# Kernel optimization log

Measured on AMD Instinct MI355X. Metric: run time of the kernel, lower is better.

## Reference

```python
import jax, jax.numpy as jnp
import numpy as np

HEAD_DIM = 64
GRID = 4
DS = 4
EPS = 1e-6


def conv1x1(x, w, b):
    # x: (B,C,H,W), w: (O,C), b: (O,)
    return jnp.einsum('bchw,oc->bohw', x, w) + b[None, :, None, None]


def setup_inputs() -> dict:
    key = jax.random.key(0)
    ks = jax.random.split(key, 12)
    B, N, C = 16, 4096, 256
    s = 0.02
    return {
        'x': jax.random.normal(ks[0], (B, N, C), dtype=jnp.float32),
        'w_qkv': s * jax.random.normal(ks[1], (3 * C, C), dtype=jnp.float32),
        'b_qkv': jnp.zeros((3 * C,), dtype=jnp.float32),
        'w_q': s * jax.random.normal(ks[2], (C, C), dtype=jnp.float32),
        'b_q': jnp.zeros((C,), dtype=jnp.float32),
        'w_kv': s * jax.random.normal(ks[3], (2 * C, C), dtype=jnp.float32),
        'b_kv': jnp.zeros((2 * C,), dtype=jnp.float32),
        'w_proj': s * jax.random.normal(ks[4], (C, C), dtype=jnp.float32),
        'b_proj': jnp.zeros((C,), dtype=jnp.float32),
        'gn_w': jnp.ones((C,), dtype=jnp.float32),
        'gn_b': jnp.zeros((C,), dtype=jnp.float32),
    }


def reference(x, w_qkv, b_qkv, w_q, b_q, w_kv, b_kv, w_proj, b_proj, gn_w, gn_b):
    B, N, C = x.shape
    H = W = int(np.sqrt(N))
    hd = HEAD_DIM
    nh = C // hd
    gs = GRID
    scale = hd ** -0.5

    xi = x.transpose(0, 2, 1).reshape(B, C, H, W)
    qkv = conv1x1(xi, w_qkv, b_qkv)  # (B,3C,H,W)

    # ---- grid-window attention (gs x gs windows) ----
    gh, gw = H // gs, W // gs
    qkv = qkv.reshape(B, 3, nh, hd, gh, gs, gw, gs)
    qkv = qkv.transpose(1, 0, 2, 4, 6, 5, 7, 3).reshape(3, -1, gs * gs, hd)
    q, k, v = qkv[0], qkv[1], qkv[2]  # (B*nh*gh*gw, gs*gs, hd)
    attn = jax.nn.softmax(jnp.einsum('wqd,wkd->wqk', q, k) * scale, axis=-1)
    grid_x = jnp.einsum('wqk,wkd->wqd', attn, v)
    grid_x = grid_x.reshape(B, nh, gh, gw, gs, gs, hd)
    grid_x = grid_x.transpose(0, 1, 6, 2, 4, 3, 5).reshape(B, C, H, W)

    # channels_first LayerNorm(x + grid_x)
    z = xi + grid_x
    u = z.mean(1, keepdims=True)
    s2 = ((z - u) ** 2).mean(1, keepdims=True)
    grid_x = gn_w[None, :, None, None] * ((z - u) / jnp.sqrt(s2 + EPS)) + gn_b[None, :, None, None]

    # ---- pooled global attention ----
    qg = conv1x1(grid_x, w_q, b_q).reshape(B, nh, hd, N).transpose(0, 1, 3, 2)  # (B,nh,N,hd)
    pooled = grid_x.reshape(B, C, H // DS, DS, W // DS, DS).mean(axis=(3, 5))
    kv = conv1x1(pooled, w_kv, b_kv).reshape(B, 2, nh, hd, -1).transpose(1, 0, 2, 4, 3)
    k, v = kv[0], kv[1]  # (B,nh,Np,hd)
    attn = jax.nn.softmax(jnp.einsum('bhqd,bhkd->bhqk', qg, k) * scale, axis=-1)
    global_x = jnp.einsum('bhqk,bhkd->bhqd', attn, v)
    global_x = global_x.transpose(0, 1, 3, 2).reshape(B, C, H, W) + grid_x

    out = conv1x1(global_x, w_proj, b_proj)
    return out.reshape(B, C, N).transpose(0, 2, 1)
```

## Files before the change

### kernel.cpp

```cpp
#include <hip/hip_runtime.h>
#include <cstddef>

#define SCALE 0.125f
#define LN_EPS 1e-6f

typedef __attribute__((ext_vector_type(8))) short bf16x8;
typedef __attribute__((ext_vector_type(4))) float f32x4;

__device__ __forceinline__ unsigned short f2bf(float f) {
    unsigned u = __float_as_uint(f);
    return (unsigned short)((u + 0x7FFFu + ((u >> 16) & 1u)) >> 16);
}
__device__ __forceinline__ unsigned pack2(float a, float b) {
    return (unsigned)f2bf(a) | ((unsigned)f2bf(b) << 16);
}
__device__ __forceinline__ float bf2f(short s) { return __uint_as_float(((unsigned)(unsigned short)s) << 16); }

#define GLOAD16(gp, lp) __builtin_amdgcn_global_load_lds( \
    (const __attribute__((address_space(1))) void*)(gp),  \
    (__attribute__((address_space(3))) void*)(lp), 16, 0, 0)

__global__ __launch_bounds__(256) void k_castw(
    const float* __restrict__ wqkv, const float* __restrict__ wq,
    const float* __restrict__ wkv, const float* __restrict__ wproj,
    short* __restrict__ wb)
{
    const int blk = blockIdx.x;
    const float* src; size_t so, doff;
    if (blk < 96)       { src = wqkv;  so = (size_t)blk * 2048;         doff = 0; }
    else if (blk < 128) { src = wq;    so = (size_t)(blk - 96) * 2048;  doff = 196608; }
    else if (blk < 192) { src = wkv;   so = (size_t)(blk - 128) * 2048; doff = 262144; }
    else                { src = wproj; so = (size_t)(blk - 192) * 2048; doff = 393216; }
    const size_t idx = so + (size_t)threadIdx.x * 8;
    const float4 f0 = *(const float4*)(src + idx);
    const float4 f1 = *(const float4*)(src + idx + 4);
    uint4 o;
    o.x = pack2(f0.x, f0.y); o.y = pack2(f0.z, f0.w);
    o.z = pack2(f1.x, f1.y); o.w = pack2(f1.z, f1.w);
    *(uint4*)(wb + doff + idx) = o;
}

__global__ __launch_bounds__(256) void k_castx(
    const float* __restrict__ x, short* __restrict__ xb)
{
    const size_t i = ((size_t)blockIdx.x * 256 + threadIdx.x) * 8;
    const float4 f0 = *(const float4*)(x + i);
    const float4 f1 = *(const float4*)(x + i + 4);
    uint4 o;
    o.x = pack2(f0.x, f0.y); o.y = pack2(f0.z, f0.w);
    o.z = pack2(f1.x, f1.y); o.w = pack2(f1.z, f1.w);
    *(uint4*)(xb + i) = o;
}

template<int OUTMODE>
__global__ __launch_bounds__(256, 4) void k_gemm(
    const short* __restrict__ Asrc, const short* __restrict__ Bw,
    const float* __restrict__ bias, void* __restrict__ Cdst,
    short* __restrict__ Vdst, int ldc, int nbn)
{
    __shared__ short Sh[17408];
    short* const As0 = Sh;
    short* const Bs0 = Sh + 8192;

    const int tid = threadIdx.x;
    const int q8 = gridDim.x >> 3;
    const int bid = (blockIdx.x & 7) * q8 + (blockIdx.x >> 3);
    const int bm = bid / nbn, bn = bid % nbn;
    const size_t m0 = (size_t)bm * 128, n0 = (size_t)bn * 128;
    const int wid = tid >> 6, lane = tid & 63;
    const int wr = wid >> 1, wc = wid & 1;
    const int g = lane >> 4, r = lane & 15;
    const int rowc = lane >> 3, gran = lane & 7;

    f32x4 acc[4][4];
    #pragma unroll
    for (int mi = 0; mi < 4; ++mi)
        #pragma unroll
        for (int nj = 0; nj < 4; ++nj) acc[mi][nj] = (f32x4)0.f;

    auto STAGE = [&](int kt) {
        const int k0 = kt * 64;
        #pragma unroll
        for (int i = 0; i < 4; ++i) {
            const int rbase = wid * 32 + i * 8;
            const int row = rbase + rowc;
            const int sg = gran ^ (row & 7);
            GLOAD16(Asrc + (m0 + row) * 256 + k0 + sg * 8, As0 + rbase * 64);
            GLOAD16(Bw   + (n0 + row) * 256 + k0 + sg * 8, Bs0 + rbase * 64);
        }
    };

    auto COMPUTE = [&]() {
        #pragma unroll
        for (int ks = 0; ks < 2; ++ks) {
            const int ke = ks * 32 + g * 8;
            bf16x8 a[4], b[4];
            #pragma unroll
            for (int mi = 0; mi < 4; ++mi) {
                const int row = wr * 64 + mi * 16 + r;
                a[mi] = *(const bf16x8*)&As0[row * 64 + (ke ^ ((row & 7) << 3))];
            }
            #pragma unroll
            for (int nj = 0; nj < 4; ++nj) {
                const int row = wc * 64 + nj * 16 + r;
                b[nj] = *(const bf16x8*)&Bs0[row * 64 + (ke ^ ((row & 7) << 3))];
            }
            #pragma unroll
            for (int mi = 0; mi < 4; ++mi)
                #pragma unroll
                for (int nj = 0; nj < 4; ++nj)
                    acc[mi][nj] = __builtin_amdgcn_mfma_f32_16x16x32_bf16(
                        a[mi], b[nj], acc[mi][nj], 0, 0, 0);
        }
    };

    #pragma unroll
    for (int kt = 0; kt < 4; ++kt) {
        STAGE(kt);
        __syncthreads();
        COMPUTE();
        __syncthreads();
    }

    if (OUTMODE == 1) {
        short* const Cl = Sh;
        #pragma unroll
        for (int nj = 0; nj < 4; ++nj) {
            const int col = wc * 64 + nj * 16 + r;
            const float bv = bias[n0 + col];
            #pragma unroll
            for (int mi = 0; mi < 4; ++mi) {
                const int row = wr * 64 + mi * 16 + g * 4;
                #pragma unroll
                for (int e = 0; e < 4; ++e)
                    Cl[(row + e) * 136 + col] = (short)f2bf(acc[mi][nj][e] + bv);
            }
        }
        __syncthreads();
        short* C = (short*)Cdst;
        #pragma unroll
        for (int j = 0; j < 8; ++j) {
            const int row = j * 16 + (tid >> 4);
            const int c8 = (tid & 15) * 8;
            const uint4 v = *(const uint4*)&Cl[row * 136 + c8];
            *(uint4*)(C + (m0 + row) * ldc + n0 + c8) = v;
        }
    } else if (OUTMODE == 0) {
        float* const Clf = (float*)Sh;
        float* C = (float*)Cdst;
        #pragma unroll
        for (int p = 0; p < 2; ++p) {
            if (wr == p) {
                #pragma unroll
                for (int nj = 0; nj < 4; ++nj) {
                    const int col = wc * 64 + nj * 16 + r;
                    const float bv = bias[n0 + col];
                    #pragma unroll
                    for (int mi = 0; mi < 4; ++mi) {
                        const int lrow = mi * 16 + g * 4;
                        #pragma unroll
                        for (int e = 0; e < 4; ++e)
                            Clf[(lrow + e) * 132 + col] = acc[mi][nj][e] + bv;
                    }
                }
            }
            __syncthreads();
            #pragma unroll
            for (int j = 0; j < 8; ++j) {
                const int lin = j * 256 + tid;
                const int row = lin >> 5, c4 = (lin & 31) * 4;
                const float4 v = *(const float4*)&Clf[row * 132 + c4];
                *(float4*)(C + (m0 + p * 64 + row) * ldc + n0 + c4) = v;
            }
            __syncthreads();
        }
    } else {
        #pragma unroll
        for (int nj = 0; nj < 4; ++nj) {
            const size_t col = n0 + wc * 64 + nj * 16 + r;
            const float bv = bias[col];
            #pragma unroll
            for (int mi = 0; mi < 4; ++mi) {
                const size_t row = m0 + wr * 64 + mi * 16 + g * 4;
                #pragma unroll
                for (int e = 0; e < 4; ++e) {
                    const float v = acc[mi][nj][e] + bv;
                    const size_t rr = row + e;
                    const int colk = (int)col - 256;
                    if (colk < 0) ((short*)Cdst)[rr * 256 + col] = (short)f2bf(v);
                    else {
                        const int hh = colk >> 6, dd = colk & 63;
                        Vdst[((((rr >> 8) * 4 + hh) * 64 + dd) << 8) + (rr & 255)] = (short)f2bf(v);
                    }
                }
            }
        }
    }
}

__global__ __launch_bounds__(256) void k_vtr(
    const short* __restrict__ qkvb, short* __restrict__ vwb)
{
    __shared__ short Vl[16][260];
    const int tid = threadIdx.x;
    const int blk = blockIdx.x;
    const int b = blk >> 8, win = blk & 255;
    const int ghi = win >> 4, gwi = win & 15;
    const size_t nb = (size_t)b * 4096;

    #pragma unroll
    for (int i = 0; i < 2; ++i) {
        const int c = i * 256 + tid;
        const int tok = c >> 5, ch = c & 31;
        const int n = (ghi * 4 + (tok >> 2)) * 64 + gwi * 4 + (tok & 3);
        const uint4 u = *(const uint4*)(qkvb + (nb + n) * 768 + 512 + ch * 8);
        short* dst = &Vl[tok][ch * 8];
        *(uint2*)dst = make_uint2(u.x, u.y);
        *(uint2*)(dst + 4) = make_uint2(u.z, u.w);
    }
    __syncthreads();

    unsigned w[8];
    #pragma unroll
    for (int k = 0; k < 8; ++k) {
        const unsigned lo = (unsigned)(unsigned short)Vl[2 * k][tid];
        const unsigned hi = (unsigned)(unsigned short)Vl[2 * k + 1][tid];
        w[k] = lo | (hi << 16);
    }
    short* dst = vwb + ((size_t)blk * 256 + tid) * 16;
    *(uint4*)dst = make_uint4(w[0], w[1], w[2], w[3]);
    *(uint4*)(dst + 8) = make_uint4(w[4], w[5], w[6], w[7]);
}

__global__ __launch_bounds__(256) void k_win3(
    const short* __restrict__ qkvb, const short* __restrict__ vwb,
    const short* __restrict__ xb, const float* __restrict__ gnw,
    const float* __restrict__ gnb, short* __restrict__ lnb,
    short* __restrict__ pooledb)
{
    __shared__ float zbuf[16][260];
    __shared__ short Pb[4][16][40];

    const int tid = threadIdx.x;
    const int blk = blockIdx.x;
    const int b = blk >> 8, win = blk & 255;
    const int ghi = win >> 4, gwi = win & 15;
    const size_t nb = (size_t)b * 4096;
    const int h = tid >> 6, lane = tid & 63;
    const int g = lane >> 4, l15 = lane & 15;

    const int n15 = (ghi * 4 + (l15 >> 2)) * 64 + gwi * 4 + (l15 & 3);
    const size_t qkrow = (nb + n15) * 768;
    const bf16x8 aq0 = *(const bf16x8*)(qkvb + qkrow + h * 64 + g * 8);
    const bf16x8 aq1 = *(const bf16x8*)(qkvb + qkrow + h * 64 + 32 + g * 8);
    const bf16x8 bk0 = *(const bf16x8*)(qkvb + qkrow + 256 + h * 64 + g * 8);
    const bf16x8 bk1 = *(const bf16x8*)(qkvb + qkrow + 256 + h * 64 + 32 + g * 8);

    f32x4 acc = (f32x4)0.f;
    acc = __builtin_amdgcn_mfma_f32_16x16x32_bf16(aq0, bk0, acc, 0, 0, 0);
    acc = __builtin_amdgcn_mfma_f32_16x16x32_bf16(aq1, bk1, acc, 0, 0, 0);

    float p[4];
    #pragma unroll
    for (int e = 0; e < 4; ++e) {
        const float s = acc[e] * SCALE;
        float mm = s;
        mm = fmaxf(mm, __shfl_xor(mm, 1)); mm = fmaxf(mm, __shfl_xor(mm, 2));
        mm = fmaxf(mm, __shfl_xor(mm, 4)); mm = fmaxf(mm, __shfl_xor(mm, 8));
        const float pe = __expf(s - mm);
        float rs = pe;
        rs += __shfl_xor(rs, 1); rs += __shfl_xor(rs, 2);
        rs += __shfl_xor(rs, 4); rs += __shfl_xor(rs, 8);
        p[e] = pe / rs;
    }
    #pragma unroll
    for (int e = 0; e < 4; ++e) {
        Pb[h][g * 4 + e][l15] = (short)f2bf(p[e]);
        Pb[h][g * 4 + e][16 + l15] = 0;
    }
    __syncthreads();

    const bf16x8 ap = *(const bf16x8*)&Pb[h][l15][g * 8];
    f32x4 oc[4];
    #pragma unroll
    for (int nt = 0; nt < 4; ++nt) oc[nt] = (f32x4)0.f;
    const short* vbase = vwb + ((((size_t)b * 256 + win) * 4 + h) << 10);
    #pragma unroll
    for (int nt = 0; nt < 4; ++nt) {
        const bf16x8 bv = *(const bf16x8*)(vbase + (nt * 16 + l15) * 16 + g * 8);
        oc[nt] = __builtin_amdgcn_mfma_f32_16x16x32_bf16(ap, bv, oc[nt], 0, 0, 0);
    }
    #pragma unroll
    for (int e = 0; e < 4; ++e)
        #pragma unroll
        for (int nt = 0; nt < 4; ++nt)
            zbuf[g * 4 + e][h * 64 + nt * 16 + l15] = oc[nt][e];
    __syncthreads();

    {
        const float4 gw = ((const float4*)gnw)[lane];
        const float4 gb = ((const float4*)gnb)[lane];
        #pragma unroll
        for (int i = 0; i < 4; ++i) {
            const int t = h * 4 + i;
            const int n = (ghi * 4 + (t >> 2)) * 64 + gwi * 4 + (t & 3);
            float4 zv = *(const float4*)&zbuf[t][lane * 4];
            const short4 xv = *(const short4*)(xb + (nb + n) * 256 + lane * 4);
            zv.x += bf2f(xv.x); zv.y += bf2f(xv.y);
            zv.z += bf2f(xv.z); zv.w += bf2f(xv.w);
            float ssum = zv.x + zv.y + zv.z + zv.w;
            for (int off = 1; off < 64; off <<= 1) ssum += __shfl_xor(ssum, off);
            const float u = ssum * (1.f / 256.f);
            const float dx = zv.x - u, dy = zv.y - u, dz = zv.z - u, dw = zv.w - u;
            float vsum = dx * dx + dy * dy + dz * dz + dw * dw;
            for (int off = 1; off < 64; off <<= 1) vsum += __shfl_xor(vsum, off);
            const float rinv = rsqrtf(vsum * (1.f / 256.f) + LN_EPS);
            float4 y;
            y.x = gw.x * dx * rinv + gb.x;
            y.y = gw.y * dy * rinv + gb.y;
            y.z = gw.z * dz * rinv + gb.z;
            y.w = gw.w * dw * rinv + gb.w;
            *(float4*)&zbuf[t][lane * 4] = y;
            short4 sv;
            sv.x = (short)f2bf(y.x); sv.y = (short)f2bf(y.y);
            sv.z = (short)f2bf(y.z); sv.w = (short)f2bf(y.w);
            *(short4*)(lnb + (nb + n) * 256 + lane * 4) = sv;
        }
    }
    __syncthreads();

    {
        float ps = 0.f;
        #pragma unroll
        for (int t = 0; t < 16; ++t) ps += zbuf[t][tid];
        pooledb[((size_t)b * 256 + win) * 256 + tid] = (short)f2bf(ps * (1.f / 16.f));
    }
}

#define CP 136
__global__ __launch_bounds__(512, 4) void k_glb(
    const short* __restrict__ qgb, const short* __restrict__ kb,
    const short* __restrict__ vtb, const short* __restrict__ lnb,
    short* __restrict__ gxb)
{
    __shared__ short Ks[128 * 64];
    __shared__ short Vt[64 * 128];
    __shared__ short Pl[8][16 * CP];

    const int tid = threadIdx.x;
    const int bid = (blockIdx.x & 7) * 256 + (blockIdx.x >> 3);
    const int bh = bid >> 5, qt = bid & 31;
    const int b = bh >> 2, h = bh & 3;
    const int q0 = qt * 128;
    const size_t nb = (size_t)b * 4096;

    const int w = tid >> 6, lane = tid & 63;
    const int g = lane >> 4, l15 = lane & 15;
    const int wbase = tid & ~63;

    bf16x8 aq[2];
    {
        const int n = q0 + w * 16 + l15;
        const short* qp = qgb + (nb + n) * 256 + h * 64 + g * 8;
        aq[0] = *(const bf16x8*)qp;
        aq[1] = *(const bf16x8*)(qp + 32);
    }

    f32x4 oc[4];
    #pragma unroll
    for (int nt = 0; nt < 4; ++nt) oc[nt] = (f32x4)0.f;
    float rs[4] = {0.f, 0.f, 0.f, 0.f};

    const short* ksrc = kb + ((size_t)b * 256) * 256 + h * 64;
    const short* vsrc = vtb + (size_t)bh * 16384;
    short* Pw = &Pl[w][0];

    for (int c = 0; c < 2; ++c) {
        if (c) __syncthreads();
        #pragma unroll
        for (int i = 0; i < 2; ++i) {
            const int cc = i * 512 + tid;
            const int p = cc >> 3;
            const int sg = (cc & 7) ^ (p & 7);
            GLOAD16(ksrc + (size_t)(c * 128 + p) * 256 + sg * 8,
                    Ks + (i * 512 + wbase) * 8);
        }
        #pragma unroll
        for (int i = 0; i < 2; ++i) {
            const int cc = i * 512 + tid;
            const int d = cc >> 4;
            const int sl = (cc & 15) ^ (d & 7);
            GLOAD16(vsrc + d * 256 + c * 128 + sl * 8,
                    Vt + (i * 512 + wbase) * 8);
        }
        __syncthreads();

        f32x4 acc[8];
        #pragma unroll
        for (int nt = 0; nt < 8; ++nt) acc[nt] = (f32x4)0.f;
        #pragma unroll
        for (int nt = 0; nt < 8; ++nt) {
            const int key = nt * 16 + l15;
            const int sw = (key & 7) << 3;
            const bf16x8 bk0 = *(const bf16x8*)&Ks[key * 64 + ((g * 8) ^ sw)];
            const bf16x8 bk1 = *(const bf16x8*)&Ks[key * 64 + ((g * 8 + 32) ^ sw)];
            acc[nt] = __builtin_amdgcn_mfma_f32_16x16x32_bf16(aq[0], bk0, acc[nt], 0, 0, 0);
            acc[nt] = __builtin_amdgcn_mfma_f32_16x16x32_bf16(aq[1], bk1, acc[nt], 0, 0, 0);
        }

        #pragma unroll
        for (int e = 0; e < 4; ++e) {
            const int prow = (g * 4 + e) * CP;
            float rsum = 0.f;
            #pragma unroll
            for (int nt = 0; nt < 8; ++nt) {
                const float p = __expf(acc[nt][e] * SCALE);
                rsum += p;
                Pw[prow + nt * 16 + l15] = (short)f2bf(p);
            }
            rs[e] += rsum;
        }

        #pragma unroll
        for (int ks = 0; ks < 4; ++ks) {
            const int kc = ks * 32 + g * 8;
            const bf16x8 a0 = *(const bf16x8*)&Pw[l15 * CP + kc];
            #pragma unroll
            for (int nt = 0; nt < 4; ++nt) {
                const int d = nt * 16 + l15;
                const bf16x8 bv = *(const bf16x8*)&Vt[d * 128 + (kc ^ ((d & 7) << 3))];
                oc[nt] = __builtin_amdgcn_mfma_f32_16x16x32_bf16(a0, bv, oc[nt], 0, 0, 0);
            }
        }
    }

    #pragma unroll
    for (int e = 0; e < 4; ++e) {
        float v = rs[e];
        v += __shfl_xor(v, 1); v += __shfl_xor(v, 2);
        v += __shfl_xor(v, 4); v += __shfl_xor(v, 8);
        rs[e] = v;
    }

    #pragma unroll
    for (int e = 0; e < 4; ++e) {
        const float inv = 1.f / rs[e];
        const int n = q0 + w * 16 + g * 4 + e;
        const size_t base = (nb + n) * 256 + h * 64;
        #pragma unroll
        for (int nt = 0; nt < 4; ++nt) {
            const int d = nt * 16 + l15;
            gxb[base + d] = (short)f2bf(oc[nt][e] * inv + bf2f(lnb[base + d]));
        }
    }
}

extern "C" void kernel_launch(void* const* d_in, const int* in_sizes, int n_in,
                              void* d_out, int out_size, void* d_ws, size_t ws_size,
                              hipStream_t stream)
{
    (void)in_sizes; (void)n_in; (void)out_size; (void)ws_size;
    const float* x     = (const float*)d_in[0];
    const float* wqkv  = (const float*)d_in[1];
    const float* bqkv  = (const float*)d_in[2];
    const float* wq    = (const float*)d_in[3];
    const float* bq    = (const float*)d_in[4];
    const float* wkv   = (const float*)d_in[5];
    const float* bkv   = (const float*)d_in[6];
    const float* wproj = (const float*)d_in[7];
    const float* bproj = (const float*)d_in[8];
    const float* gnw   = (const float*)d_in[9];
    const float* gnb   = (const float*)d_in[10];
    float* out = (float*)d_out;

    char* wsb = (char*)d_ws;
    short* wb      = (short*)(wsb + 0);
    short* qkvb    = (short*)(wsb + 1048576);
    short* lnb     = (short*)(wsb + 101711872);
    short* qgb     = (short*)(wsb + 135266304);
    short* kb      = (short*)(wsb + 168820736);
    short* vtb     = (short*)(wsb + 170917888);
    short* pooledb = (short*)(wsb + 173015040);
    short* gxb     = (short*)(wsb + 175112192);
    short* vwb     = gxb;
    short* xb      = (short*)(wsb + 208666624);

    k_castw<<<dim3(224),  dim3(256), 0, stream>>>(wqkv, wq, wkv, wproj, wb);
    k_castx<<<dim3(8192), dim3(256), 0, stream>>>(x, xb);
    k_gemm<1><<<dim3(3072), dim3(256), 0, stream>>>(xb, wb, bqkv, qkvb, nullptr, 768, 6);
    k_vtr<<<dim3(4096), dim3(256), 0, stream>>>(qkvb, vwb);
    k_win3<<<dim3(4096), dim3(256), 0, stream>>>(qkvb, vwb, xb, gnw, gnb, lnb, pooledb);
    k_gemm<1><<<dim3(1024), dim3(256), 0, stream>>>(lnb, wb + 196608, bq, qgb, nullptr, 256, 2);
    k_gemm<2><<<dim3(128), dim3(256), 0, stream>>>(pooledb, wb + 262144, bkv, kb, vtb, 512, 4);
    k_glb<<<dim3(2048), dim3(512), 0, stream>>>(qgb, kb, vtb, lnb, gxb);
    k_gemm<0><<<dim3(1024), dim3(256), 0, stream>>>(gxb, wb + 393216, bproj, out, nullptr, 256, 2);
}
```

Before: 193.5 us.

## Keep softmax probabilities in registers via transposed QK MFMA and lane shuffles

Swaps the MFMA operand order for the QK^T product so each lane holds scores for one query across four keys. The probabilities are then packed to bf16 with a hardware convert and redistributed to the PV MFMA A-operand layout with lane shuffles, instead of a round trip through a per-wave LDS scratch buffer. This removes the P shared buffer, which lowers LDS usage and drops the write/read traffic, and simplifies the row-sum reduction. The cost is extra cross-lane shuffles and selects per k-step.

```diff
diff --git a/kernel.cpp b/kernel.cpp
--- a/kernel.cpp
+++ b/kernel.cpp
@@ -6,6 +6,7 @@
 
 typedef __attribute__((ext_vector_type(8))) short bf16x8;
 typedef __attribute__((ext_vector_type(4))) float f32x4;
+typedef __attribute__((ext_vector_type(4))) unsigned u32x4;
 
 __device__ __forceinline__ unsigned short f2bf(float f) {
     unsigned u = __float_as_uint(f);
@@ -15,6 +16,11 @@
     return (unsigned)f2bf(a) | ((unsigned)f2bf(b) << 16);
 }
 __device__ __forceinline__ float bf2f(short s) { return __uint_as_float(((unsigned)(unsigned short)s) << 16); }
+__device__ __forceinline__ unsigned cvtpk(float lo, float hi) {
+    unsigned r;
+    asm("v_cvt_pk_bf16_f32 %0, %1, %2" : "=v"(r) : "v"(lo), "v"(hi));
+    return r;
+}
 
 #define GLOAD16(gp, lp) __builtin_amdgcn_global_load_lds( \
     (const __attribute__((address_space(1))) void*)(gp),  \
@@ -337,7 +343,6 @@
     }
 }
 
-#define CP 136
 __global__ __launch_bounds__(512, 4) void k_glb(
     const short* __restrict__ qgb, const short* __restrict__ kb,
     const short* __restrict__ vtb, const short* __restrict__ lnb,
@@ -345,7 +350,6 @@
 {
     __shared__ short Ks[128 * 64];
     __shared__ short Vt[64 * 128];
-    __shared__ short Pl[8][16 * CP];
 
     const int tid = threadIdx.x;
     const int bid = (blockIdx.x & 7) * 256 + (blockIdx.x >> 3);
@@ -369,11 +373,14 @@
     f32x4 oc[4];
     #pragma unroll
     for (int nt = 0; nt < 4; ++nt) oc[nt] = (f32x4)0.f;
-    float rs[4] = {0.f, 0.f, 0.f, 0.f};
+    float rst = 0.f;
 
     const short* ksrc = kb + ((size_t)b * 256) * 256 + h * 64;
     const short* vsrc = vtb + (size_t)bh * 16384;
-    short* Pw = &Pl[w][0];
+
+    const int s0 = ((g & 1) << 5) | l15;
+    const int s1 = s0 | 16;
+    const bool hi = (g >> 1) != 0;
 
     for (int c = 0; c < 2; ++c) {
         if (c) __syncthreads();
@@ -404,47 +411,55 @@
             const int sw = (key & 7) << 3;
             const bf16x8 bk0 = *(const bf16x8*)&Ks[key * 64 + ((g * 8) ^ sw)];
             const bf16x8 bk1 = *(const bf16x8*)&Ks[key * 64 + ((g * 8 + 32) ^ sw)];
-            acc[nt] = __builtin_amdgcn_mfma_f32_16x16x32_bf16(aq[0], bk0, acc[nt], 0, 0, 0);
-            acc[nt] = __builtin_amdgcn_mfma_f32_16x16x32_bf16(aq[1], bk1, acc[nt], 0, 0, 0);
-        }
-
-        #pragma unroll
-        for (int e = 0; e < 4; ++e) {
-            const int prow = (g * 4 + e) * CP;
-            float rsum = 0.f;
-            #pragma unroll
-            for (int nt = 0; nt < 8; ++nt) {
-                const float p = __expf(acc[nt][e] * SCALE);
-                rsum += p;
-                Pw[prow + nt * 16 + l15] = (short)f2bf(p);
-            }
-            rs[e] += rsum;
+            acc[nt] = __builtin_amdgcn_mfma_f32_16x16x32_bf16(bk0, aq[0], acc[nt], 0, 0, 0);
+            acc[nt] = __builtin_amdgcn_mfma_f32_16x16x32_bf16(bk1, aq[1], acc[nt], 0, 0, 0);
+        }
+
+        unsigned pk0[8], pk1[8];
+        #pragma unroll
+        for (int nt = 0; nt < 8; ++nt) {
+            const float p0 = __expf(acc[nt][0] * SCALE);
+            const float p1 = __expf(acc[nt][1] * SCALE);
+            const float p2 = __expf(acc[nt][2] * SCALE);
+            const float p3 = __expf(acc[nt][3] * SCALE);
+            rst += (p0 + p1) + (p2 + p3);
+            pk0[nt] = cvtpk(p0, p1);
+            pk1[nt] = cvtpk(p2, p3);
         }
 
         #pragma unroll
         for (int ks = 0; ks < 4; ++ks) {
+            const unsigned a0 = (unsigned)__shfl((int)pk0[2 * ks],     s0);
+            const unsigned b0 = (unsigned)__shfl((int)pk0[2 * ks + 1], s0);
+            const unsigned a1 = (unsigned)__shfl((int)pk1[2 * ks],     s0);
+            const unsigned b1 = (unsigned)__shfl((int)pk1[2 * ks + 1], s0);
+            const unsigned a2 = (unsigned)__shfl((int)pk0[2 * ks],     s1);
+            const unsigned b2 = (unsigned)__shfl((int)pk0[2 * ks + 1], s1);
+            const unsigned a3 = (unsigned)__shfl((int)pk1[2 * ks],     s1);
+            const unsigned b3 = (unsigned)__shfl((int)pk1[2 * ks + 1], s1);
+            u32x4 aw;
+            aw.x = hi ? b0 : a0;
+            aw.y = hi ? b1 : a1;
+            aw.z = hi ? b2 : a2;
+            aw.w = hi ? b3 : a3;
+            const bf16x8 af = __builtin_bit_cast(bf16x8, aw);
             const int kc = ks * 32 + g * 8;
-            const bf16x8 a0 = *(const bf16x8*)&Pw[l15 * CP + kc];
             #pragma unroll
             for (int nt = 0; nt < 4; ++nt) {
                 const int d = nt * 16 + l15;
                 const bf16x8 bv = *(const bf16x8*)&Vt[d * 128 + (kc ^ ((d & 7) << 3))];
-                oc[nt] = __builtin_amdgcn_mfma_f32_16x16x32_bf16(a0, bv, oc[nt], 0, 0, 0);
-            }
-        }
-    }
+                oc[nt] = __builtin_amdgcn_mfma_f32_16x16x32_bf16(af, bv, oc[nt], 0, 0, 0);
+            }
+        }
+    }
+
+    rst += __shfl_xor(rst, 16);
+    rst += __shfl_xor(rst, 32);
 
     #pragma unroll
     for (int e = 0; e < 4; ++e) {
-        float v = rs[e];
-        v += __shfl_xor(v, 1); v += __shfl_xor(v, 2);
-        v += __shfl_xor(v, 4); v += __shfl_xor(v, 8);
-        rs[e] = v;
-    }
-
-    #pragma unroll
-    for (int e = 0; e < 4; ++e) {
-        const float inv = 1.f / rs[e];
+        const float rq = __shfl(rst, g * 4 + e);
+        const float inv = 1.f / rq;
         const int n = q0 + w * 16 + g * 4 + e;
         const size_t base = (nb + n) * 256 + h * 64;
         #pragma unroll
```

Result: no change. 194.7 us (+0.6%).
